# Kernel optimization log

Measured on AMD Instinct MI355X. Metric: run time of the kernel, lower is better.

## Reference

```python
import jax, jax.numpy as jnp
import numpy as np

B, P = 16, 4096            # clouds, points per cloud (N = B*P)
RATIO = 0.25
M = int(P * RATIO)          # FPS samples per cloud = 1024
K = 16                      # num_neighbors
F_IN, F_OUT = 64, 128
BN_EPS = 1e-5


def setup_inputs() -> dict:
    key = jax.random.key(0)
    k1, k2, k3 = jax.random.split(key, 3)
    position = jax.random.normal(k1, (B * P, 3), jnp.float32)
    features = jax.random.normal(k2, (B * P, F_IN), jnp.float32)
    batch_indices = jnp.repeat(jnp.arange(B, dtype=jnp.int32), P)  # sorted, equal-sized clouds
    W = jax.random.normal(k3, (F_IN, F_OUT), jnp.float32) * 0.05
    b = jnp.zeros((F_OUT,), jnp.float32)
    gamma = jnp.ones((F_OUT,), jnp.float32)
    beta = jnp.zeros((F_OUT,), jnp.float32)
    return {"position": position, "features": features, "batch_indices": batch_indices,
            "W": W, "b": b, "gamma": gamma, "beta": beta}


def _fps(pos):
    """Farthest point sampling on one cloud. pos: [P,3] -> indices [M].
    Deterministic start at index 0 (torch_cluster uses a random start)."""
    def step(carry, _):
        dist, last = carry
        d = jnp.sum((pos - pos[last]) ** 2, axis=-1)      # [P]
        dist = jnp.minimum(dist, d)                        # min dist to selected set
        nxt = jnp.argmax(dist).astype(jnp.int32)
        return (dist, nxt), nxt
    init = (jnp.full((P,), jnp.inf, pos.dtype), jnp.int32(0))
    _, idx = jax.lax.scan(step, init, None, length=M - 1)
    return jnp.concatenate([jnp.zeros((1,), jnp.int32), idx])


def _knn(x, q):
    """k nearest neighbors of queries q [M,F] among x [P,F] (feature space!). -> [M,K] indices."""
    d2 = (jnp.sum(q * q, -1, keepdims=True) - 2.0 * q @ x.T + jnp.sum(x * x, -1))  # [M,P]
    _, idx = jax.lax.top_k(-d2, K)
    return idx


def reference(position, features, batch_indices, W, b, gamma, beta):
    pos = position.reshape(B, P, 3)
    feat = features.reshape(B, P, F_IN)

    # FPS on positions (per cloud)
    fps_idx = jax.vmap(_fps)(pos)                                   # [B,M]

    # MLP: Linear + BatchNorm1d (training-mode batch stats over all N) + ReLU
    h = features @ W + b                                            # [N,F_OUT]
    mean = jnp.mean(h, axis=0)
    var = jnp.var(h, axis=0)
    h = jax.nn.relu((h - mean) * jax.lax.rsqrt(var + BN_EPS) * gamma + beta)
    h = h.reshape(B, P, F_OUT)

    # KNN in feature space: queries are features at FPS indices
    q = jnp.take_along_axis(feat, fps_idx[..., None], axis=1)       # [B,M,F_IN]
    nbr = jax.vmap(_knn)(feat, q)                                   # [B,M,K]

    # gather transformed features of neighbors and max-pool per query
    nbr_feats = jax.vmap(lambda hb, ib: hb[ib])(h, nbr)             # [B,M,K,F_OUT]
    new_features = jnp.max(nbr_feats, axis=2).reshape(B * M, F_OUT)

    new_position = jnp.take_along_axis(pos, fps_idx[..., None], axis=1).reshape(B * M, 3)
    new_batch = jnp.repeat(jnp.arange(B, dtype=batch_indices.dtype), M)
    return new_features, new_position, new_batch
```

## Files before the change

### kernel.cpp

```cpp
#include <hip/hip_runtime.h>
#include <hip/hip_bf16.h>

#define NB 16
#define NP 4096
#define MS 1024
#define NN 65536
#define FIN 64
#define FOUT 128
#define KNN_MARGIN 0.25f

typedef __attribute__((ext_vector_type(8))) short short8;
typedef __attribute__((ext_vector_type(4))) float f32x4;
typedef __attribute__((ext_vector_type(2))) float f32x2;

template <int CTRL>
__device__ __forceinline__ unsigned long long dpp_fmax_step(unsigned long long k) {
    unsigned lo = (unsigned)k, hi = (unsigned)(k >> 32);
    unsigned plo = (unsigned)__builtin_amdgcn_update_dpp(0, (int)lo, CTRL, 0xf, 0xf, true);
    unsigned phi = (unsigned)__builtin_amdgcn_update_dpp(0, (int)hi, CTRL, 0xf, 0xf, true);
    unsigned long long pk = ((unsigned long long)phi << 32) | plo;
    double a = __builtin_bit_cast(double, k);
    double p = __builtin_bit_cast(double, pk);
    return __builtin_bit_cast(unsigned long long, fmax(a, p));
}

__device__ __forceinline__ unsigned short bf16_rn(float v) {
    unsigned u = __float_as_uint(v);
    unsigned r = u + 0x7FFF + ((u >> 16) & 1);
    return (unsigned short)(r >> 16);
}


__global__ __launch_bounds__(512, 1) void front_kernel(
        const float* __restrict__ pos, const float* __restrict__ feat,
        const float* __restrict__ W, const float* __restrict__ bias,
        int* __restrict__ fps_idx, float* __restrict__ out_pos, float* __restrict__ out_batch,
        float* __restrict__ xnorm, unsigned short* __restrict__ Xt,
        __hip_bfloat16* __restrict__ hout, float* __restrict__ gsum, float* __restrict__ gsq) {
    __shared__ __align__(16) char smraw[69760];
    const int t = threadIdx.x;
    const int b = blockIdx.x;
    if (b < 16) {
        float4* plds4 = (float4*)smraw;
        float*  plin  = (float*)smraw;
        int* idxL = (int*)(smraw + 65536);
        double* wk = (double*)(smraw + 65536 + 4096);
        const float* pb = pos + (size_t)b * NP * 3;
#pragma unroll
        for (int i = 0; i < 24; i++) { int id = t + 512 * i; plin[id] = pb[id]; }
        __syncthreads();
        f32x2 px2[4], py2[4], pz2[4], dist2[4];
#pragma unroll
        for (int j = 0; j < 4; j++) {
            int p0 = t + 512 * (2 * j), p1 = p0 + 512;
            px2[j] = {plin[p0 * 3 + 0], plin[p1 * 3 + 0]};
            py2[j] = {plin[p0 * 3 + 1], plin[p1 * 3 + 1]};
            pz2[j] = {plin[p0 * 3 + 2], plin[p1 * 3 + 2]};
            dist2[j] = {INFINITY, INFINITY};
        }
        __syncthreads();
#pragma unroll
        for (int j = 0; j < 4; j++) {
            plds4[t + 512 * (2 * j)]     = (float4){px2[j][0], py2[j][0], pz2[j][0], 0.f};
            plds4[t + 512 * (2 * j + 1)] = (float4){px2[j][1], py2[j][1], pz2[j][1], 0.f};
        }
        if (t == 0) idxL[0] = 0;
        __syncthreads();
        float4 c0 = plds4[0];
        float lx = c0.x, ly = c0.y, lz = c0.z;
        const int ln = t & 63, wv = t >> 6;
        for (int m = 1; m < MS; m++) {
#pragma unroll
            for (int j = 0; j < 4; j++) {
                f32x2 dx = px2[j] - lx, dy = py2[j] - ly, dz = pz2[j] - lz;
                f32x2 d = dx * dx + dy * dy + dz * dz;
                dist2[j] = __builtin_elementwise_min(dist2[j], d);
            }
            float d1[4]; int i1[4];
#pragma unroll
            for (int j = 0; j < 4; j++) {
                bool g = dist2[j][1] > dist2[j][0];
                d1[j] = g ? dist2[j][1] : dist2[j][0];
                i1[j] = 2 * j + (g ? 1 : 0);
            }
            float d2[2]; int i2[2];
#pragma unroll
            for (int j = 0; j < 2; j++) {
                bool g = d1[j + 2] > d1[j];
                d2[j] = g ? d1[j + 2] : d1[j]; i2[j] = g ? i1[j + 2] : i1[j];
            }
            bool g3 = d2[1] > d2[0];
            float bd = g3 ? d2[1] : d2[0];
            int bi = g3 ? i2[1] : i2[0];
            int bp = t + (bi << 9);
            unsigned long long key =
                ((unsigned long long)__float_as_uint(bd) << 32) | (unsigned)(~bp);
            key = dpp_fmax_step<0x111>(key);
            key = dpp_fmax_step<0x112>(key);
            key = dpp_fmax_step<0x114>(key);
            key = dpp_fmax_step<0x118>(key);
            key = dpp_fmax_step<0x142>(key);
            key = dpp_fmax_step<0x143>(key);
            const int par = (m & 1) * 8;
            if (ln == 63) wk[par + wv] = __builtin_bit_cast(double, key);
            __syncthreads();
            const double2* wk2 = (const double2*)(wk + par);
            double2 q01 = wk2[0], q23 = wk2[1], q45 = wk2[2], q67 = wk2[3];
            double ka = fmax(q01.x, q01.y), kb = fmax(q23.x, q23.y);
            double kc = fmax(q45.x, q45.y), kd = fmax(q67.x, q67.y);
            ka = fmax(ka, kb);
            kc = fmax(kc, kd);
            unsigned long long kw = __builtin_bit_cast(unsigned long long, fmax(ka, kc));
            bp = (int)(~(unsigned)kw) & 0xFFF;
            float4 c = plds4[bp];
            lx = c.x; ly = c.y; lz = c.z;
            if (t == 0) idxL[m] = bp;
        }
        __syncthreads();
        for (int m = t; m < MS; m += 512) {
            int ix = idxL[m];
            size_t o = (size_t)b * MS + m;
            fps_idx[o] = ix;
            float4 c = plds4[ix];
            out_pos[o * 3 + 0] = c.x;
            out_pos[o * 3 + 1] = c.y;
            out_pos[o * 3 + 2] = c.z;
            out_batch[o] = (float)b;
        }
    } else if (b < 272) {
        float* wt = (float*)smraw;
        float* fl = (float*)smraw + 8704;
#pragma unroll
        for (int it = 0; it < 4; it++) {
            int lid = t + 512 * it;
            int k = lid >> 5, c4 = lid & 31;
            float4 v = *(const float4*)&W[k * FOUT + c4 * 4];
            wt[(c4 * 4 + 0) * 68 + k] = v.x;
            wt[(c4 * 4 + 1) * 68 + k] = v.y;
            wt[(c4 * 4 + 2) * 68 + k] = v.z;
            wt[(c4 * 4 + 3) * 68 + k] = v.w;
        }
        const int rowbase0 = (b - 16) * 256;
        const int rg = t >> 5, cg = t & 31;
        float sums[4] = {0, 0, 0, 0};
        float sqs[4]  = {0, 0, 0, 0};
        for (int sub = 0; sub < 4; sub++) {
            const int rowbase = rowbase0 + sub * 64;
            __syncthreads();
#pragma unroll
            for (int it = 0; it < 2; it++) {
                int lid = t + 512 * it;
                int r = lid >> 4, f4 = lid & 15;
                float4 v = *(const float4*)&feat[(size_t)(rowbase + r) * FIN + f4 * 4];
                *(float4*)&fl[r * 68 + f4 * 4] = v;
            }
            __syncthreads();
            float acc[4][4];
#pragma unroll
            for (int i = 0; i < 4; i++)
#pragma unroll
                for (int j = 0; j < 4; j++) acc[i][j] = 0.f;
#pragma unroll 2
            for (int k4 = 0; k4 < 16; k4++) {
                float4 f4v[4], w4v[4];
#pragma unroll
                for (int i = 0; i < 4; i++) f4v[i] = *(float4*)&fl[(rg * 4 + i) * 68 + k4 * 4];
#pragma unroll
                for (int j = 0; j < 4; j++) w4v[j] = *(float4*)&wt[(cg + 32 * j) * 68 + k4 * 4];
#pragma unroll
                for (int i = 0; i < 4; i++)
#pragma unroll
                    for (int j = 0; j < 4; j++) {
                        acc[i][j] = fmaf(f4v[i].x, w4v[j].x, acc[i][j]);
                        acc[i][j] = fmaf(f4v[i].y, w4v[j].y, acc[i][j]);
                        acc[i][j] = fmaf(f4v[i].z, w4v[j].z, acc[i][j]);
                        acc[i][j] = fmaf(f4v[i].w, w4v[j].w, acc[i][j]);
                    }
            }
#pragma unroll
            for (int j = 0; j < 4; j++) {
                int c = cg + 32 * j;
                float bc = bias[c];
#pragma unroll
                for (int i = 0; i < 4; i++) {
                    float h = acc[i][j] + bc;
                    sums[j] += h; sqs[j] += h * h;
                    hout[(size_t)(rowbase + rg * 4 + i) * FOUT + c] = __float2bfloat16(h);
                }
            }
        }
        __syncthreads();
        float* suml = fl;
        float* sql  = wt;
#pragma unroll
        for (int j = 0; j < 4; j++) {
            suml[rg * FOUT + cg + 32 * j] = sums[j];
            sql[rg * FOUT + cg + 32 * j]  = sqs[j];
        }
        __syncthreads();
        if (t < FOUT) {
            float S = 0.f, Q = 0.f;
#pragma unroll
            for (int r = 0; r < 16; r++) { S += suml[r * FOUT + t]; Q += sql[r * FOUT + t]; }
            atomicAdd(&gsum[t], S);
            atomicAdd(&gsq[t], Q);
        }
    } else {
        int r = (b - 272) * 512 + t;
        const float4* fr = (const float4*)&feat[(size_t)r * FIN];
        unsigned short hrow[64], lrow[64];
        float s = 0.f;
#pragma unroll
        for (int i = 0; i < 16; i++) {
            float4 v = fr[i];
            s += v.x * v.x + v.y * v.y + v.z * v.z + v.w * v.w;
            float vv[4] = {v.x, v.y, v.z, v.w};
#pragma unroll
            for (int j = 0; j < 4; j++) {
                unsigned short h = bf16_rn(vv[j]);
                float hf = __uint_as_float((unsigned)h << 16);
                hrow[4 * i + j] = h;
                lrow[4 * i + j] = bf16_rn(vv[j] - hf);
            }
        }
        xnorm[r] = s;
        const size_t tbase = (size_t)(r >> 4) * 2048;
        const int col = r & 15;
#pragma unroll
        for (int q = 0; q < 4; q++) {
            short8 f0, f1, f2, f3;
#pragma unroll
            for (int j = 0; j < 8; j++) {
                f0[j] = (short)hrow[q * 8 + j];
                f1[j] = (short)hrow[32 + q * 8 + j];
                f2[j] = (short)lrow[q * 8 + j];
                f3[j] = (short)lrow[32 + q * 8 + j];
            }
            const int ch = (q * 16 + col) * 8;
            *(short8*)&Xt[tbase + ch]        = f0;
            *(short8*)&Xt[tbase + 512 + ch]  = f1;
            *(short8*)&Xt[tbase + 1024 + ch] = f2;
            *(short8*)&Xt[tbase + 1536 + ch] = f3;
        }
    }
}

#define KNN_LOAD(SLOT_H0, SLOT_H1, SLOT_L0, SLOT_L1, SLOT_XN, TILE)                     \
    {                                                                                   \
        const unsigned short* tb_ = Xt + (size_t)(gtbase + (TILE)) * 2048;              \
        SLOT_H0 = *(const short8*)(tb_ + lane * 8);                                     \
        SLOT_H1 = *(const short8*)(tb_ + 512 + lane * 8);                               \
        SLOT_L0 = *(const short8*)(tb_ + 1024 + lane * 8);                              \
        SLOT_L1 = *(const short8*)(tb_ + 1536 + lane * 8);                              \
        SLOT_XN = xnorm[cbase + pstart + (TILE) * 16 + col];                            \
    }

#define KNN_MFMA(ACC, H0, H1, L0, L1)                                                   \
    ACC = __builtin_amdgcn_mfma_f32_16x16x32_bf16(Ah0, H0, ACC, 0, 0, 0);               \
    ACC = __builtin_amdgcn_mfma_f32_16x16x32_bf16(Ah1, H1, ACC, 0, 0, 0);               \
    ACC = __builtin_amdgcn_mfma_f32_16x16x32_bf16(Al0, H0, ACC, 0, 0, 0);               \
    ACC = __builtin_amdgcn_mfma_f32_16x16x32_bf16(Al1, H1, ACC, 0, 0, 0);               \
    ACC = __builtin_amdgcn_mfma_f32_16x16x32_bf16(Ah0, L0, ACC, 0, 0, 0);               \
    ACC = __builtin_amdgcn_mfma_f32_16x16x32_bf16(Ah1, L1, ACC, 0, 0, 0);

__global__ __launch_bounds__(256, 2) void knn_kernel(
        const unsigned short* __restrict__ Xt,
        const int* __restrict__ fps_idx, const float* __restrict__ xnorm,
        unsigned short* __restrict__ cand) {
    __shared__ float TL[4][16][32];
    __shared__ float TQ[4][16];
    __shared__ int   cntL[4][16];
    __shared__ unsigned short buf[4][16][64];
    const int t = threadIdx.x, b = blockIdx.x;
    const int cloud = b & 15, qg = (b >> 4) & 15, half = b >> 8;
    const int wave = t >> 6, lane = t & 63;
    const int quad = lane >> 4, col = lane & 15;
    const int cbase = cloud * NP;
    const int qloc = qg * 64 + wave * 16;
    const int pstart = half * 2048;
    const int gtbase = cloud * 256 + half * 128;

    const int qrow = fps_idx[cloud * MS + qloc + col];
    const unsigned short* qt = Xt + (size_t)(cloud * 256 + (qrow >> 4)) * 2048
                               + (size_t)((quad << 4) | (qrow & 15)) * 8;
    short8 Ah0 = *(const short8*)(qt);
    short8 Ah1 = *(const short8*)(qt + 512);
    short8 Al0 = *(const short8*)(qt + 1024);
    short8 Al1 = *(const short8*)(qt + 1536);

    float mA[4] = {INFINITY, INFINITY, INFINITY, INFINITY};
    float mB[4] = {INFINITY, INFINITY, INFINITY, INFINITY};
    {
        short8 ah0, ah1, al0, al1; float axn;
        short8 bh0, bh1, bl0, bl1; float bxn;
        KNN_LOAD(ah0, ah1, al0, al1, axn, 0)
        KNN_LOAD(bh0, bh1, bl0, bl1, bxn, 1)
        for (int tt = 0; tt < 128; tt += 2) {
            {
                f32x4 acc = {0.f, 0.f, 0.f, 0.f};
                KNN_MFMA(acc, ah0, ah1, al0, al1)
                float xnv = axn;
                if (tt + 2 < 128) KNN_LOAD(ah0, ah1, al0, al1, axn, tt + 2)
#pragma unroll
                for (int r = 0; r < 4; r++) {
                    float s = fmaf(-2.0f, acc[r], xnv);
                    float mx = fmaxf(mA[r], s);
                    mA[r] = fminf(mA[r], s);
                    mB[r] = fminf(mB[r], mx);
                }
            }
            {
                f32x4 acc = {0.f, 0.f, 0.f, 0.f};
                KNN_MFMA(acc, bh0, bh1, bl0, bl1)
                float xnv = bxn;
                if (tt + 3 < 128) KNN_LOAD(bh0, bh1, bl0, bl1, bxn, tt + 3)
#pragma unroll
                for (int r = 0; r < 4; r++) {
                    float s = fmaf(-2.0f, acc[r], xnv);
                    float mx = fmaxf(mA[r], s);
                    mA[r] = fminf(mA[r], s);
                    mB[r] = fminf(mB[r], mx);
                }
            }
        }
    }
#pragma unroll
    for (int r = 0; r < 4; r++) {
        TL[wave][quad * 4 + r][col * 2 + 0] = mA[r];
        TL[wave][quad * 4 + r][col * 2 + 1] = mB[r];
    }
    if (lane < 16) cntL[wave][lane] = 0;
    {
        const int q = lane >> 2, j0 = (lane & 3) * 8;
        float v[32];
#pragma unroll
        for (int j = 0; j < 32; j++) v[j] = TL[wave][q][j];
#pragma unroll
        for (int u = 0; u < 8; u++) {
            float vj = TL[wave][q][j0 + u];
            int jj = j0 + u, rank = 0;
#pragma unroll
            for (int k = 0; k < 32; k++)
                rank += (v[k] < vj || (v[k] == vj && k < jj)) ? 1 : 0;
            if (rank == 15) TQ[wave][q] = vj;
        }
    }
    float T0 = TQ[wave][quad * 4 + 0] + KNN_MARGIN;
    float T1 = TQ[wave][quad * 4 + 1] + KNN_MARGIN;
    float T2 = TQ[wave][quad * 4 + 2] + KNN_MARGIN;
    float T3 = TQ[wave][quad * 4 + 3] + KNN_MARGIN;
    {
        short8 ah0, ah1, al0, al1; float axn;
        short8 bh0, bh1, bl0, bl1; float bxn;
        KNN_LOAD(ah0, ah1, al0, al1, axn, 0)
        KNN_LOAD(bh0, bh1, bl0, bl1, bxn, 1)
        for (int tt = 0; tt < 128; tt += 2) {
            {
                f32x4 acc = {0.f, 0.f, 0.f, 0.f};
                KNN_MFMA(acc, ah0, ah1, al0, al1)
                float xnv = axn;
                if (tt + 2 < 128) KNN_LOAD(ah0, ah1, al0, al1, axn, tt + 2)
                const int pidx = pstart + tt * 16 + col;
                float s0 = fmaf(-2.0f, acc[0], xnv);
                float s1 = fmaf(-2.0f, acc[1], xnv);
                float s2 = fmaf(-2.0f, acc[2], xnv);
                float s3 = fmaf(-2.0f, acc[3], xnv);
                if (s0 <= T0) { int p = atomicAdd(&cntL[wave][quad * 4 + 0], 1); if (p < 64) buf[wave][quad * 4 + 0][p] = (unsigned short)pidx; }
                if (s1 <= T1) { int p = atomicAdd(&cntL[wave][quad * 4 + 1], 1); if (p < 64) buf[wave][quad * 4 + 1][p] = (unsigned short)pidx; }
                if (s2 <= T2) { int p = atomicAdd(&cntL[wave][quad * 4 + 2], 1); if (p < 64) buf[wave][quad * 4 + 2][p] = (unsigned short)pidx; }
                if (s3 <= T3) { int p = atomicAdd(&cntL[wave][quad * 4 + 3], 1); if (p < 64) buf[wave][quad * 4 + 3][p] = (unsigned short)pidx; }
            }
            {
                f32x4 acc = {0.f, 0.f, 0.f, 0.f};
                KNN_MFMA(acc, bh0, bh1, bl0, bl1)
                float xnv = bxn;
                if (tt + 3 < 128) KNN_LOAD(bh0, bh1, bl0, bl1, bxn, tt + 3)
                const int pidx = pstart + (tt + 1) * 16 + col;
                float s0 = fmaf(-2.0f, acc[0], xnv);
                float s1 = fmaf(-2.0f, acc[1], xnv);
                float s2 = fmaf(-2.0f, acc[2], xnv);
                float s3 = fmaf(-2.0f, acc[3], xnv);
                if (s0 <= T0) { int p = atomicAdd(&cntL[wave][quad * 4 + 0], 1); if (p < 64) buf[wave][quad * 4 + 0][p] = (unsigned short)pidx; }
                if (s1 <= T1) { int p = atomicAdd(&cntL[wave][quad * 4 + 1], 1); if (p < 64) buf[wave][quad * 4 + 1][p] = (unsigned short)pidx; }
                if (s2 <= T2) { int p = atomicAdd(&cntL[wave][quad * 4 + 2], 1); if (p < 64) buf[wave][quad * 4 + 2][p] = (unsigned short)pidx; }
                if (s3 <= T3) { int p = atomicAdd(&cntL[wave][quad * 4 + 3], 1); if (p < 64) buf[wave][quad * 4 + 3][p] = (unsigned short)pidx; }
            }
        }
    }
#pragma unroll
    for (int q = 0; q < 16; q++) {
        int n = cntL[wave][q];
        unsigned short val = (lane < n) ? buf[wave][q][lane] : (unsigned short)0xFFFF;
        cand[(size_t)(cloud * MS + qloc + q) * 128 + half * 64 + lane] = val;
    }
}

__global__ __launch_bounds__(256) void refine_kernel(
        const float* __restrict__ feat, const int* __restrict__ fps_idx,
        const float* __restrict__ xnorm, const unsigned short* __restrict__ cand,
        const __hip_bfloat16* __restrict__ h,
        const float* __restrict__ gsum, const float* __restrict__ gsq,
        const float* __restrict__ gamma, const float* __restrict__ beta,
        float* __restrict__ out_feat) {
    __shared__ float qlds[64];
    __shared__ __align__(16) int2 cDI[128];
    __shared__ int   rankH[128];
    __shared__ int   fIdx[16];
    __shared__ float cf[256];
    __shared__ float pmax[128];
    const int t = threadIdx.x, b = blockIdx.x;
    const int cloud = b & 15, m = b >> 4;
    const int q = cloud * MS + m;
    const int cbase = cloud * NP;
    if (t < 128) {
        float mean = gsum[t] * (1.0f / NN);
        float var  = gsq[t] * (1.0f / NN) - mean * mean;
        float s = rsqrtf(var + 1e-5f) * gamma[t];
        cf[t] = s;
        cf[128 + t] = beta[t] - mean * s;
    }
    if (t < 16) {
        int qr = fps_idx[q];
        float4 v = ((const float4*)(feat + (size_t)(cbase + qr) * FIN))[t];
        *(float4*)&qlds[t * 4] = v;
    }
    __syncthreads();
    const int c = t >> 1, jh = t & 1;
    const unsigned short cs = cand[(size_t)q * 128 + c];
    const bool valid = (cs != 0xFFFF);
    const int cidx = valid ? (int)cs : 0;
    const float4* xr = (const float4*)(feat + (size_t)(cbase + cidx) * FIN) + jh * 8;
    float a0 = 0.f, a1 = 0.f, a2 = 0.f, a3 = 0.f;
#pragma unroll
    for (int i = 0; i < 8; i++) {
        float4 x4 = xr[i];
        a0 = fmaf(qlds[jh * 32 + 4 * i + 0], x4.x, a0);
        a1 = fmaf(qlds[jh * 32 + 4 * i + 1], x4.y, a1);
        a2 = fmaf(qlds[jh * 32 + 4 * i + 2], x4.z, a2);
        a3 = fmaf(qlds[jh * 32 + 4 * i + 3], x4.w, a3);
    }
    float a = (a0 + a1) + (a2 + a3);
    a += __shfl_xor(a, 1);
    if (jh == 0) {
        float dv = valid ? fmaf(-2.0f, a, xnorm[cbase + cidx]) : INFINITY;
        int   iv = valid ? cidx : (65536 + c);
        cDI[c] = make_int2(__float_as_int(dv), iv);
    }
    __syncthreads();
    {
        const int c2 = t & 127, jH = t >> 7;
        int2 my = cDI[c2];
        float dv = __int_as_float(my.x);
        int   iv = my.y;
        const int4* cDI4 = (const int4*)cDI;
        int rank = 0;
        const int base = jH * 32;
#pragma unroll 8
        for (int k2 = 0; k2 < 32; k2++) {
            int4 p = cDI4[base + k2];
            float d0 = __int_as_float(p.x); int i0 = p.y;
            float d1 = __int_as_float(p.z); int i1 = p.w;
            rank += (d0 < dv || (d0 == dv && i0 < iv)) ? 1 : 0;
            rank += (d1 < dv || (d1 == dv && i1 < iv)) ? 1 : 0;
        }
        if (jH) rankH[c2] = rank;
        __syncthreads();
        if (!jH) {
            rank += rankH[c2];
            if (rank < 16) fIdx[rank] = iv;
        }
    }
    __syncthreads();
    {
        const int tc = t & 127, kH = t >> 7;
        const __hip_bfloat16* hb = h + (size_t)cbase * FOUT;
        const float ac = cf[tc], cc = cf[128 + tc];
        float mx = -INFINITY;
#pragma unroll
        for (int k = 0; k < 8; k++) {
            int row = fIdx[kH * 8 + k];
            float hv = __bfloat162float(hb[(size_t)row * FOUT + tc]);
            mx = fmaxf(mx, fmaxf(fmaf(ac, hv, cc), 0.f));
        }
        if (kH) pmax[tc] = mx;
        __syncthreads();
        if (!kH) out_feat[(size_t)q * FOUT + tc] = fmaxf(mx, pmax[tc]);
    }
}

extern "C" void kernel_launch(void* const* d_in, const int* in_sizes, int n_in,
                              void* d_out, int out_size, void* d_ws, size_t ws_size,
                              hipStream_t stream) {
    (void)in_sizes; (void)n_in; (void)out_size; (void)ws_size;
    const float* position = (const float*)d_in[0];
    const float* features = (const float*)d_in[1];
    const float* W        = (const float*)d_in[3];
    const float* bias     = (const float*)d_in[4];
    const float* gamma    = (const float*)d_in[5];
    const float* beta     = (const float*)d_in[6];
    float* out = (float*)d_out;

    char* ws = (char*)d_ws;
    int*   fps_idx = (int*)ws;
    float* gsum    = (float*)(ws + 65536);
    float* gsq     = (float*)(ws + 66048);
    float* xnorm   = (float*)(ws + 67584);
    unsigned short* cand = (unsigned short*)(ws + 329728);
    unsigned short* Xt   = (unsigned short*)(ws + 4524032);
    __hip_bfloat16* hbuf = (__hip_bfloat16*)(ws + 21301248);

    float* out_feat  = out;
    float* out_pos   = out + 2097152;
    float* out_batch = out + 2146304;

    hipMemsetAsync(gsum, 0, 1024, stream);
    front_kernel<<<400, 512, 0, stream>>>(position, features, W, bias,
                                          fps_idx, out_pos, out_batch, xnorm, Xt,
                                          hbuf, gsum, gsq);
    knn_kernel<<<512, 256, 0, stream>>>(Xt, fps_idx, xnorm, cand);
    refine_kernel<<<16384, 256, 0, stream>>>(features, fps_idx, xnorm, cand,
                                             hbuf, gsum, gsq, gamma, beta, out_feat);
}
```

Before: 759.0 us.

## Fuse front and KNN kernels with FPS progress flags to overlap KNN with FPS

Merges the FPS/MLP/split-bf16 front kernel and the KNN candidate kernel into one persistent launch of 256 blocks. The 16 FPS blocks publish selected indices every 64 samples through agent-scope release flags. The other blocks first build Xt and run the MLP tiles, then start KNN query tasks as soon as the matching FPS prefix is ready. This hides the serial FPS latency behind KNN and MLP work instead of running KNN only after it ends. The cost is spin-waiting on global flags and a reliance on all 256 blocks being co-resident to avoid deadlock.

```diff
diff --git a/kernel.cpp b/kernel.cpp
--- a/kernel.cpp
+++ b/kernel.cpp
@@ -31,12 +31,31 @@
 }
 
 
-__global__ __launch_bounds__(512, 1) void front_kernel(
+#define KNN_LOAD(SLOT_H0, SLOT_H1, SLOT_L0, SLOT_L1, SLOT_XN, TILE)                     \
+    {                                                                                   \
+        const unsigned short* tb_ = Xt + (size_t)(gtbase + (TILE)) * 2048;              \
+        SLOT_H0 = *(const short8*)(tb_ + lane * 8);                                     \
+        SLOT_H1 = *(const short8*)(tb_ + 512 + lane * 8);                               \
+        SLOT_L0 = *(const short8*)(tb_ + 1024 + lane * 8);                              \
+        SLOT_L1 = *(const short8*)(tb_ + 1536 + lane * 8);                              \
+        SLOT_XN = xnorm[cbase + pstart + (TILE) * 16 + col];                            \
+    }
+
+#define KNN_MFMA(ACC, H0, H1, L0, L1)                                                   \
+    ACC = __builtin_amdgcn_mfma_f32_16x16x32_bf16(Ah0, H0, ACC, 0, 0, 0);               \
+    ACC = __builtin_amdgcn_mfma_f32_16x16x32_bf16(Ah1, H1, ACC, 0, 0, 0);               \
+    ACC = __builtin_amdgcn_mfma_f32_16x16x32_bf16(Al0, H0, ACC, 0, 0, 0);               \
+    ACC = __builtin_amdgcn_mfma_f32_16x16x32_bf16(Al1, H1, ACC, 0, 0, 0);               \
+    ACC = __builtin_amdgcn_mfma_f32_16x16x32_bf16(Ah0, L0, ACC, 0, 0, 0);               \
+    ACC = __builtin_amdgcn_mfma_f32_16x16x32_bf16(Ah1, L1, ACC, 0, 0, 0);
+
+__global__ __launch_bounds__(512) void fused_kernel(
         const float* __restrict__ pos, const float* __restrict__ feat,
         const float* __restrict__ W, const float* __restrict__ bias,
         int* __restrict__ fps_idx, float* __restrict__ out_pos, float* __restrict__ out_batch,
         float* __restrict__ xnorm, unsigned short* __restrict__ Xt,
-        __hip_bfloat16* __restrict__ hout, float* __restrict__ gsum, float* __restrict__ gsq) {
+        __hip_bfloat16* __restrict__ hout, float* __restrict__ gsum, float* __restrict__ gsq,
+        unsigned short* __restrict__ cand, int* __restrict__ ready, int* __restrict__ sdone) {
     __shared__ __align__(16) char smraw[69760];
     const int t = threadIdx.x;
     const int b = blockIdx.x;
@@ -64,7 +83,7 @@
             plds4[t + 512 * (2 * j)]     = (float4){px2[j][0], py2[j][0], pz2[j][0], 0.f};
             plds4[t + 512 * (2 * j + 1)] = (float4){px2[j][1], py2[j][1], pz2[j][1], 0.f};
         }
-        if (t == 0) idxL[0] = 0;
+        if (t == 0) { idxL[0] = 0; fps_idx[(size_t)b * MS] = 0; }
         __syncthreads();
         float4 c0 = plds4[0];
         float lx = c0.x, ly = c0.y, lz = c0.z;
@@ -114,284 +133,284 @@
             bp = (int)(~(unsigned)kw) & 0xFFF;
             float4 c = plds4[bp];
             lx = c.x; ly = c.y; lz = c.z;
-            if (t == 0) idxL[m] = bp;
+            if (t == 0) {
+                idxL[m] = bp;
+                fps_idx[(size_t)b * MS + m] = bp;
+                if ((m & 63) == 63) {
+                    __threadfence();
+                    __hip_atomic_store(&ready[b], m + 1, __ATOMIC_RELEASE,
+                                       __HIP_MEMORY_SCOPE_AGENT);
+                }
+            }
         }
         __syncthreads();
         for (int m = t; m < MS; m += 512) {
             int ix = idxL[m];
             size_t o = (size_t)b * MS + m;
-            fps_idx[o] = ix;
             float4 c = plds4[ix];
             out_pos[o * 3 + 0] = c.x;
             out_pos[o * 3 + 1] = c.y;
             out_pos[o * 3 + 2] = c.z;
             out_batch[o] = (float)b;
         }
-    } else if (b < 272) {
-        float* wt = (float*)smraw;
-        float* fl = (float*)smraw + 8704;
-#pragma unroll
-        for (int it = 0; it < 4; it++) {
-            int lid = t + 512 * it;
-            int k = lid >> 5, c4 = lid & 31;
-            float4 v = *(const float4*)&W[k * FOUT + c4 * 4];
-            wt[(c4 * 4 + 0) * 68 + k] = v.x;
-            wt[(c4 * 4 + 1) * 68 + k] = v.y;
-            wt[(c4 * 4 + 2) * 68 + k] = v.z;
-            wt[(c4 * 4 + 3) * 68 + k] = v.w;
-        }
-        const int rowbase0 = (b - 16) * 256;
-        const int rg = t >> 5, cg = t & 31;
-        float sums[4] = {0, 0, 0, 0};
-        float sqs[4]  = {0, 0, 0, 0};
-        for (int sub = 0; sub < 4; sub++) {
-            const int rowbase = rowbase0 + sub * 64;
+    } else {
+        const int w = b - 16;
+        if (w < 128) {
+            int r = w * 512 + t;
+            const float4* fr = (const float4*)&feat[(size_t)r * FIN];
+            unsigned short hrow[64], lrow[64];
+            float s = 0.f;
+#pragma unroll
+            for (int i = 0; i < 16; i++) {
+                float4 v = fr[i];
+                s += v.x * v.x + v.y * v.y + v.z * v.z + v.w * v.w;
+                float vv[4] = {v.x, v.y, v.z, v.w};
+#pragma unroll
+                for (int j = 0; j < 4; j++) {
+                    unsigned short h = bf16_rn(vv[j]);
+                    float hf = __uint_as_float((unsigned)h << 16);
+                    hrow[4 * i + j] = h;
+                    lrow[4 * i + j] = bf16_rn(vv[j] - hf);
+                }
+            }
+            xnorm[r] = s;
+            const size_t tbase = (size_t)(r >> 4) * 2048;
+            const int col = r & 15;
+#pragma unroll
+            for (int q = 0; q < 4; q++) {
+                short8 f0, f1, f2, f3;
+#pragma unroll
+                for (int j = 0; j < 8; j++) {
+                    f0[j] = (short)hrow[q * 8 + j];
+                    f1[j] = (short)hrow[32 + q * 8 + j];
+                    f2[j] = (short)lrow[q * 8 + j];
+                    f3[j] = (short)lrow[32 + q * 8 + j];
+                }
+                const int ch = (q * 16 + col) * 8;
+                *(short8*)&Xt[tbase + ch]        = f0;
+                *(short8*)&Xt[tbase + 512 + ch]  = f1;
+                *(short8*)&Xt[tbase + 1024 + ch] = f2;
+                *(short8*)&Xt[tbase + 1536 + ch] = f3;
+            }
+            __threadfence();
+        }
+        __syncthreads();
+        if (w < 128 && t == 0)
+            __hip_atomic_fetch_add(sdone, 1, __ATOMIC_RELEASE, __HIP_MEMORY_SCOPE_AGENT);
+        for (int tile = w; tile < 256; tile += 240) {
+            float* wt = (float*)smraw;
+            float* fl = (float*)smraw + 8704;
+#pragma unroll
+            for (int it = 0; it < 4; it++) {
+                int lid = t + 512 * it;
+                int k = lid >> 5, c4 = lid & 31;
+                float4 v = *(const float4*)&W[k * FOUT + c4 * 4];
+                wt[(c4 * 4 + 0) * 68 + k] = v.x;
+                wt[(c4 * 4 + 1) * 68 + k] = v.y;
+                wt[(c4 * 4 + 2) * 68 + k] = v.z;
+                wt[(c4 * 4 + 3) * 68 + k] = v.w;
+            }
+            const int rowbase0 = tile * 256;
+            const int rg = t >> 5, cg = t & 31;
+            float sums[4] = {0, 0, 0, 0};
+            float sqs[4]  = {0, 0, 0, 0};
+            for (int sub = 0; sub < 4; sub++) {
+                const int rowbase = rowbase0 + sub * 64;
+                __syncthreads();
+#pragma unroll
+                for (int it = 0; it < 2; it++) {
+                    int lid = t + 512 * it;
+                    int r = lid >> 4, f4 = lid & 15;
+                    float4 v = *(const float4*)&feat[(size_t)(rowbase + r) * FIN + f4 * 4];
+                    *(float4*)&fl[r * 68 + f4 * 4] = v;
+                }
+                __syncthreads();
+                float acc[4][4];
+#pragma unroll
+                for (int i = 0; i < 4; i++)
+#pragma unroll
+                    for (int j = 0; j < 4; j++) acc[i][j] = 0.f;
+#pragma unroll 2
+                for (int k4 = 0; k4 < 16; k4++) {
+                    float4 f4v[4], w4v[4];
+#pragma unroll
+                    for (int i = 0; i < 4; i++) f4v[i] = *(float4*)&fl[(rg * 4 + i) * 68 + k4 * 4];
+#pragma unroll
+                    for (int j = 0; j < 4; j++) w4v[j] = *(float4*)&wt[(cg + 32 * j) * 68 + k4 * 4];
+#pragma unroll
+                    for (int i = 0; i < 4; i++)
+#pragma unroll
+                        for (int j = 0; j < 4; j++) {
+                            acc[i][j] = fmaf(f4v[i].x, w4v[j].x, acc[i][j]);
+                            acc[i][j] = fmaf(f4v[i].y, w4v[j].y, acc[i][j]);
+                            acc[i][j] = fmaf(f4v[i].z, w4v[j].z, acc[i][j]);
+                            acc[i][j] = fmaf(f4v[i].w, w4v[j].w, acc[i][j]);
+                        }
+                }
+#pragma unroll
+                for (int j = 0; j < 4; j++) {
+                    int c = cg + 32 * j;
+                    float bc = bias[c];
+#pragma unroll
+                    for (int i = 0; i < 4; i++) {
+                        float h = acc[i][j] + bc;
+                        sums[j] += h; sqs[j] += h * h;
+                        hout[(size_t)(rowbase + rg * 4 + i) * FOUT + c] = __float2bfloat16(h);
+                    }
+                }
+            }
             __syncthreads();
-#pragma unroll
-            for (int it = 0; it < 2; it++) {
-                int lid = t + 512 * it;
-                int r = lid >> 4, f4 = lid & 15;
-                float4 v = *(const float4*)&feat[(size_t)(rowbase + r) * FIN + f4 * 4];
-                *(float4*)&fl[r * 68 + f4 * 4] = v;
+            float* suml = fl;
+            float* sql  = wt;
+#pragma unroll
+            for (int j = 0; j < 4; j++) {
+                suml[rg * FOUT + cg + 32 * j] = sums[j];
+                sql[rg * FOUT + cg + 32 * j]  = sqs[j];
             }
             __syncthreads();
-            float acc[4][4];
-#pragma unroll
-            for (int i = 0; i < 4; i++)
-#pragma unroll
-                for (int j = 0; j < 4; j++) acc[i][j] = 0.f;
-#pragma unroll 2
-            for (int k4 = 0; k4 < 16; k4++) {
-                float4 f4v[4], w4v[4];
-#pragma unroll
-                for (int i = 0; i < 4; i++) f4v[i] = *(float4*)&fl[(rg * 4 + i) * 68 + k4 * 4];
-#pragma unroll
-                for (int j = 0; j < 4; j++) w4v[j] = *(float4*)&wt[(cg + 32 * j) * 68 + k4 * 4];
-#pragma unroll
-                for (int i = 0; i < 4; i++)
-#pragma unroll
-                    for (int j = 0; j < 4; j++) {
-                        acc[i][j] = fmaf(f4v[i].x, w4v[j].x, acc[i][j]);
-                        acc[i][j] = fmaf(f4v[i].y, w4v[j].y, acc[i][j]);
-                        acc[i][j] = fmaf(f4v[i].z, w4v[j].z, acc[i][j]);
-                        acc[i][j] = fmaf(f4v[i].w, w4v[j].w, acc[i][j]);
+            if (t < FOUT) {
+                float S = 0.f, Q = 0.f;
+#pragma unroll
+                for (int r = 0; r < 16; r++) { S += suml[r * FOUT + t]; Q += sql[r * FOUT + t]; }
+                atomicAdd(&gsum[t], S);
+                atomicAdd(&gsq[t], Q);
+            }
+            __syncthreads();
+        }
+        float (*TL)[16][32] = (float(*)[16][32])smraw;
+        float (*TQ)[16]     = (float(*)[16])(smraw + 16384);
+        int   (*cntL)[16]   = (int(*)[16])(smraw + 16896);
+        unsigned short (*bufL)[16][64] = (unsigned short(*)[16][64])(smraw + 17408);
+        const int wave = t >> 6, lane = t & 63;
+        const int quad = lane >> 4, col = lane & 15;
+        while (__hip_atomic_load(sdone, __ATOMIC_ACQUIRE, __HIP_MEMORY_SCOPE_AGENT) < 128)
+            __builtin_amdgcn_s_sleep(64);
+        auto knn_task = [&](int tid) {
+            const int cloud = tid & 15;
+            const int half  = (tid >> 4) & 1;
+            const int qloc  = (tid >> 5) * 16;
+            const int cbase = cloud * NP;
+            const int pstart = half * 2048;
+            const int gtbase = cloud * 256 + half * 128;
+            const int need = qloc + 16;
+            while (__hip_atomic_load(&ready[cloud], __ATOMIC_ACQUIRE,
+                                     __HIP_MEMORY_SCOPE_AGENT) < need)
+                __builtin_amdgcn_s_sleep(64);
+            const int qrow = fps_idx[cloud * MS + qloc + col];
+            const unsigned short* qt = Xt + (size_t)(cloud * 256 + (qrow >> 4)) * 2048
+                                       + (size_t)((quad << 4) | (qrow & 15)) * 8;
+            short8 Ah0 = *(const short8*)(qt);
+            short8 Ah1 = *(const short8*)(qt + 512);
+            short8 Al0 = *(const short8*)(qt + 1024);
+            short8 Al1 = *(const short8*)(qt + 1536);
+            float mA[4] = {INFINITY, INFINITY, INFINITY, INFINITY};
+            float mB[4] = {INFINITY, INFINITY, INFINITY, INFINITY};
+            {
+                short8 ah0, ah1, al0, al1; float axn;
+                short8 bh0, bh1, bl0, bl1; float bxn;
+                KNN_LOAD(ah0, ah1, al0, al1, axn, 0)
+                KNN_LOAD(bh0, bh1, bl0, bl1, bxn, 1)
+                for (int tt = 0; tt < 128; tt += 2) {
+                    {
+                        f32x4 acc = {0.f, 0.f, 0.f, 0.f};
+                        KNN_MFMA(acc, ah0, ah1, al0, al1)
+                        float xnv = axn;
+                        if (tt + 2 < 128) KNN_LOAD(ah0, ah1, al0, al1, axn, tt + 2)
+#pragma unroll
+                        for (int r = 0; r < 4; r++) {
+                            float s = fmaf(-2.0f, acc[r], xnv);
+                            float mx = fmaxf(mA[r], s);
+                            mA[r] = fminf(mA[r], s);
+                            mB[r] = fminf(mB[r], mx);
+                        }
                     }
-            }
-#pragma unroll
-            for (int j = 0; j < 4; j++) {
-                int c = cg + 32 * j;
-                float bc = bias[c];
-#pragma unroll
-                for (int i = 0; i < 4; i++) {
-                    float h = acc[i][j] + bc;
-                    sums[j] += h; sqs[j] += h * h;
-                    hout[(size_t)(rowbase + rg * 4 + i) * FOUT + c] = __float2bfloat16(h);
-                }
-            }
-        }
-        __syncthreads();
-        float* suml = fl;
-        float* sql  = wt;
-#pragma unroll
-        for (int j = 0; j < 4; j++) {
-            suml[rg * FOUT + cg + 32 * j] = sums[j];
-            sql[rg * FOUT + cg + 32 * j]  = sqs[j];
-        }
-        __syncthreads();
-        if (t < FOUT) {
-            float S = 0.f, Q = 0.f;
-#pragma unroll
-            for (int r = 0; r < 16; r++) { S += suml[r * FOUT + t]; Q += sql[r * FOUT + t]; }
-            atomicAdd(&gsum[t], S);
-            atomicAdd(&gsq[t], Q);
-        }
-    } else {
-        int r = (b - 272) * 512 + t;
-        const float4* fr = (const float4*)&feat[(size_t)r * FIN];
-        unsigned short hrow[64], lrow[64];
-        float s = 0.f;
-#pragma unroll
-        for (int i = 0; i < 16; i++) {
-            float4 v = fr[i];
-            s += v.x * v.x + v.y * v.y + v.z * v.z + v.w * v.w;
-            float vv[4] = {v.x, v.y, v.z, v.w};
-#pragma unroll
-            for (int j = 0; j < 4; j++) {
-                unsigned short h = bf16_rn(vv[j]);
-                float hf = __uint_as_float((unsigned)h << 16);
-                hrow[4 * i + j] = h;
-                lrow[4 * i + j] = bf16_rn(vv[j] - hf);
-            }
-        }
-        xnorm[r] = s;
-        const size_t tbase = (size_t)(r >> 4) * 2048;
-        const int col = r & 15;
-#pragma unroll
-        for (int q = 0; q < 4; q++) {
-            short8 f0, f1, f2, f3;
-#pragma unroll
-            for (int j = 0; j < 8; j++) {
-                f0[j] = (short)hrow[q * 8 + j];
-                f1[j] = (short)hrow[32 + q * 8 + j];
-                f2[j] = (short)lrow[q * 8 + j];
-                f3[j] = (short)lrow[32 + q * 8 + j];
-            }
-            const int ch = (q * 16 + col) * 8;
-            *(short8*)&Xt[tbase + ch]        = f0;
-            *(short8*)&Xt[tbase + 512 + ch]  = f1;
-            *(short8*)&Xt[tbase + 1024 + ch] = f2;
-            *(short8*)&Xt[tbase + 1536 + ch] = f3;
-        }
-    }
-}
-
-#define KNN_LOAD(SLOT_H0, SLOT_H1, SLOT_L0, SLOT_L1, SLOT_XN, TILE)                     \
-    {                                                                                   \
-        const unsigned short* tb_ = Xt + (size_t)(gtbase + (TILE)) * 2048;              \
-        SLOT_H0 = *(const short8*)(tb_ + lane * 8);                                     \
-        SLOT_H1 = *(const short8*)(tb_ + 512 + lane * 8);                               \
-        SLOT_L0 = *(const short8*)(tb_ + 1024 + lane * 8);                              \
-        SLOT_L1 = *(const short8*)(tb_ + 1536 + lane * 8);                              \
-        SLOT_XN = xnorm[cbase + pstart + (TILE) * 16 + col];                            \
-    }
-
-#define KNN_MFMA(ACC, H0, H1, L0, L1)                                                   \
-    ACC = __builtin_amdgcn_mfma_f32_16x16x32_bf16(Ah0, H0, ACC, 0, 0, 0);               \
-    ACC = __builtin_amdgcn_mfma_f32_16x16x32_bf16(Ah1, H1, ACC, 0, 0, 0);               \
-    ACC = __builtin_amdgcn_mfma_f32_16x16x32_bf16(Al0, H0, ACC, 0, 0, 0);               \
-    ACC = __builtin_amdgcn_mfma_f32_16x16x32_bf16(Al1, H1, ACC, 0, 0, 0);               \
-    ACC = __builtin_amdgcn_mfma_f32_16x16x32_bf16(Ah0, L0, ACC, 0, 0, 0);               \
-    ACC = __builtin_amdgcn_mfma_f32_16x16x32_bf16(Ah1, L1, ACC, 0, 0, 0);
-
-__global__ __launch_bounds__(256, 2) void knn_kernel(
-        const unsigned short* __restrict__ Xt,
-        const int* __restrict__ fps_idx, const float* __restrict__ xnorm,
-        unsigned short* __restrict__ cand) {
-    __shared__ float TL[4][16][32];
-    __shared__ float TQ[4][16];
-    __shared__ int   cntL[4][16];
-    __shared__ unsigned short buf[4][16][64];
-    const int t = threadIdx.x, b = blockIdx.x;
-    const int cloud = b & 15, qg = (b >> 4) & 15, half = b >> 8;
-    const int wave = t >> 6, lane = t & 63;
-    const int quad = lane >> 4, col = lane & 15;
-    const int cbase = cloud * NP;
-    const int qloc = qg * 64 + wave * 16;
-    const int pstart = half * 2048;
-    const int gtbase = cloud * 256 + half * 128;
-
-    const int qrow = fps_idx[cloud * MS + qloc + col];
-    const unsigned short* qt = Xt + (size_t)(cloud * 256 + (qrow >> 4)) * 2048
-                               + (size_t)((quad << 4) | (qrow & 15)) * 8;
-    short8 Ah0 = *(const short8*)(qt);
-    short8 Ah1 = *(const short8*)(qt + 512);
-    short8 Al0 = *(const short8*)(qt + 1024);
-    short8 Al1 = *(const short8*)(qt + 1536);
-
-    float mA[4] = {INFINITY, INFINITY, INFINITY, INFINITY};
-    float mB[4] = {INFINITY, INFINITY, INFINITY, INFINITY};
-    {
-        short8 ah0, ah1, al0, al1; float axn;
-        short8 bh0, bh1, bl0, bl1; float bxn;
-        KNN_LOAD(ah0, ah1, al0, al1, axn, 0)
-        KNN_LOAD(bh0, bh1, bl0, bl1, bxn, 1)
-        for (int tt = 0; tt < 128; tt += 2) {
+                    {
+                        f32x4 acc = {0.f, 0.f, 0.f, 0.f};
+                        KNN_MFMA(acc, bh0, bh1, bl0, bl1)
+                        float xnv = bxn;
+                        if (tt + 3 < 128) KNN_LOAD(bh0, bh1, bl0, bl1, bxn, tt + 3)
+#pragma unroll
+                        for (int r = 0; r < 4; r++) {
+                            float s = fmaf(-2.0f, acc[r], xnv);
+                            float mx = fmaxf(mA[r], s);
+                            mA[r] = fminf(mA[r], s);
+                            mB[r] = fminf(mB[r], mx);
+                        }
+                    }
+                }
+            }
+#pragma unroll
+            for (int r = 0; r < 4; r++) {
+                TL[wave][quad * 4 + r][col * 2 + 0] = mA[r];
+                TL[wave][quad * 4 + r][col * 2 + 1] = mB[r];
+            }
+            if (lane < 16) cntL[wave][lane] = 0;
             {
-                f32x4 acc = {0.f, 0.f, 0.f, 0.f};
-                KNN_MFMA(acc, ah0, ah1, al0, al1)
-                float xnv = axn;
-                if (tt + 2 < 128) KNN_LOAD(ah0, ah1, al0, al1, axn, tt + 2)
-#pragma unroll
-                for (int r = 0; r < 4; r++) {
-                    float s = fmaf(-2.0f, acc[r], xnv);
-                    float mx = fmaxf(mA[r], s);
-                    mA[r] = fminf(mA[r], s);
-                    mB[r] = fminf(mB[r], mx);
-                }
-            }
+                const int q = lane >> 2, j0 = (lane & 3) * 8;
+                float v[32];
+#pragma unroll
+                for (int j = 0; j < 32; j++) v[j] = TL[wave][q][j];
+#pragma unroll
+                for (int u = 0; u < 8; u++) {
+                    float vj = TL[wave][q][j0 + u];
+                    int jj = j0 + u, rank = 0;
+#pragma unroll
+                    for (int k = 0; k < 32; k++)
+                        rank += (v[k] < vj || (v[k] == vj && k < jj)) ? 1 : 0;
+                    if (rank == 15) TQ[wave][q] = vj;
+                }
+            }
+            float T0 = TQ[wave][quad * 4 + 0] + KNN_MARGIN;
+            float T1 = TQ[wave][quad * 4 + 1] + KNN_MARGIN;
+            float T2 = TQ[wave][quad * 4 + 2] + KNN_MARGIN;
+            float T3 = TQ[wave][quad * 4 + 3] + KNN_MARGIN;
             {
-                f32x4 acc = {0.f, 0.f, 0.f, 0.f};
-                KNN_MFMA(acc, bh0, bh1, bl0, bl1)
-                float xnv = bxn;
-                if (tt + 3 < 128) KNN_LOAD(bh0, bh1, bl0, bl1, bxn, tt + 3)
-#pragma unroll
-                for (int r = 0; r < 4; r++) {
-                    float s = fmaf(-2.0f, acc[r], xnv);
-                    float mx = fmaxf(mA[r], s);
-                    mA[r] = fminf(mA[r], s);
-                    mB[r] = fminf(mB[r], mx);
-                }
-            }
-        }
-    }
-#pragma unroll
-    for (int r = 0; r < 4; r++) {
-        TL[wave][quad * 4 + r][col * 2 + 0] = mA[r];
-        TL[wave][quad * 4 + r][col * 2 + 1] = mB[r];
-    }
-    if (lane < 16) cntL[wave][lane] = 0;
-    {
-        const int q = lane >> 2, j0 = (lane & 3) * 8;
-        float v[32];
-#pragma unroll
-        for (int j = 0; j < 32; j++) v[j] = TL[wave][q][j];
-#pragma unroll
-        for (int u = 0; u < 8; u++) {
-            float vj = TL[wave][q][j0 + u];
-            int jj = j0 + u, rank = 0;
-#pragma unroll
-            for (int k = 0; k < 32; k++)
-                rank += (v[k] < vj || (v[k] == vj && k < jj)) ? 1 : 0;
-            if (rank == 15) TQ[wave][q] = vj;
-        }
-    }
-    float T0 = TQ[wave][quad * 4 + 0] + KNN_MARGIN;
-    float T1 = TQ[wave][quad * 4 + 1] + KNN_MARGIN;
-    float T2 = TQ[wave][quad * 4 + 2] + KNN_MARGIN;
-    float T3 = TQ[wave][quad * 4 + 3] + KNN_MARGIN;
-    {
-        short8 ah0, ah1, al0, al1; float axn;
-        short8 bh0, bh1, bl0, bl1; float bxn;
-        KNN_LOAD(ah0, ah1, al0, al1, axn, 0)
-        KNN_LOAD(bh0, bh1, bl0, bl1, bxn, 1)
-        for (int tt = 0; tt < 128; tt += 2) {
-            {
-                f32x4 acc = {0.f, 0.f, 0.f, 0.f};
-                KNN_MFMA(acc, ah0, ah1, al0, al1)
-                float xnv = axn;
-                if (tt + 2 < 128) KNN_LOAD(ah0, ah1, al0, al1, axn, tt + 2)
-                const int pidx = pstart + tt * 16 + col;
-                float s0 = fmaf(-2.0f, acc[0], xnv);
-                float s1 = fmaf(-2.0f, acc[1], xnv);
-                float s2 = fmaf(-2.0f, acc[2], xnv);
-                float s3 = fmaf(-2.0f, acc[3], xnv);
-                if (s0 <= T0) { int p = atomicAdd(&cntL[wave][quad * 4 + 0], 1); if (p < 64) buf[wave][quad * 4 + 0][p] = (unsigned short)pidx; }
-                if (s1 <= T1) { int p = atomicAdd(&cntL[wave][quad * 4 + 1], 1); if (p < 64) buf[wave][quad * 4 + 1][p] = (unsigned short)pidx; }
-                if (s2 <= T2) { int p = atomicAdd(&cntL[wave][quad * 4 + 2], 1); if (p < 64) buf[wave][quad * 4 + 2][p] = (unsigned short)pidx; }
-                if (s3 <= T3) { int p = atomicAdd(&cntL[wave][quad * 4 + 3], 1); if (p < 64) buf[wave][quad * 4 + 3][p] = (unsigned short)pidx; }
-            }
-            {
-                f32x4 acc = {0.f, 0.f, 0.f, 0.f};
-                KNN_MFMA(acc, bh0, bh1, bl0, bl1)
-                float xnv = bxn;
-                if (tt + 3 < 128) KNN_LOAD(bh0, bh1, bl0, bl1, bxn, tt + 3)
-                const int pidx = pstart + (tt + 1) * 16 + col;
-                float s0 = fmaf(-2.0f, acc[0], xnv);
-                float s1 = fmaf(-2.0f, acc[1], xnv);
-                float s2 = fmaf(-2.0f, acc[2], xnv);
-                float s3 = fmaf(-2.0f, acc[3], xnv);
-                if (s0 <= T0) { int p = atomicAdd(&cntL[wave][quad * 4 + 0], 1); if (p < 64) buf[wave][quad * 4 + 0][p] = (unsigned short)pidx; }
-                if (s1 <= T1) { int p = atomicAdd(&cntL[wave][quad * 4 + 1], 1); if (p < 64) buf[wave][quad * 4 + 1][p] = (unsigned short)pidx; }
-                if (s2 <= T2) { int p = atomicAdd(&cntL[wave][quad * 4 + 2], 1); if (p < 64) buf[wave][quad * 4 + 2][p] = (unsigned short)pidx; }
-                if (s3 <= T3) { int p = atomicAdd(&cntL[wave][quad * 4 + 3], 1); if (p < 64) buf[wave][quad * 4 + 3][p] = (unsigned short)pidx; }
-            }
-        }
-    }
-#pragma unroll
-    for (int q = 0; q < 16; q++) {
-        int n = cntL[wave][q];
-        unsigned short val = (lane < n) ? buf[wave][q][lane] : (unsigned short)0xFFFF;
-        cand[(size_t)(cloud * MS + qloc + q) * 128 + half * 64 + lane] = val;
+                short8 ah0, ah1, al0, al1; float axn;
+                short8 bh0, bh1, bl0, bl1; float bxn;
+                KNN_LOAD(ah0, ah1, al0, al1, axn, 0)
+                KNN_LOAD(bh0, bh1, bl0, bl1, bxn, 1)
+                for (int tt = 0; tt < 128; tt += 2) {
+                    {
+                        f32x4 acc = {0.f, 0.f, 0.f, 0.f};
+                        KNN_MFMA(acc, ah0, ah1, al0, al1)
+                        float xnv = axn;
+                        if (tt + 2 < 128) KNN_LOAD(ah0, ah1, al0, al1, axn, tt + 2)
+                        const int pidx = pstart + tt * 16 + col;
+                        float s0 = fmaf(-2.0f, acc[0], xnv);
+                        float s1 = fmaf(-2.0f, acc[1], xnv);
+                        float s2 = fmaf(-2.0f, acc[2], xnv);
+                        float s3 = fmaf(-2.0f, acc[3], xnv);
+                        if (s0 <= T0) { int p = atomicAdd(&cntL[wave][quad * 4 + 0], 1); if (p < 64) bufL[wave][quad * 4 + 0][p] = (unsigned short)pidx; }
+                        if (s1 <= T1) { int p = atomicAdd(&cntL[wave][quad * 4 + 1], 1); if (p < 64) bufL[wave][quad * 4 + 1][p] = (unsigned short)pidx; }
+                        if (s2 <= T2) { int p = atomicAdd(&cntL[wave][quad * 4 + 2], 1); if (p < 64) bufL[wave][quad * 4 + 2][p] = (unsigned short)pidx; }
+                        if (s3 <= T3) { int p = atomicAdd(&cntL[wave][quad * 4 + 3], 1); if (p < 64) bufL[wave][quad * 4 + 3][p] = (unsigned short)pidx; }
+                    }
+                    {
+                        f32x4 acc = {0.f, 0.f, 0.f, 0.f};
+                        KNN_MFMA(acc, bh0, bh1, bl0, bl1)
+                        float xnv = bxn;
+                        if (tt + 3 < 128) KNN_LOAD(bh0, bh1, bl0, bl1, bxn, tt + 3)
+                        const int pidx = pstart + (tt + 1) * 16 + col;
+                        float s0 = fmaf(-2.0f, acc[0], xnv);
+                        float s1 = fmaf(-2.0f, acc[1], xnv);
+                        float s2 = fmaf(-2.0f, acc[2], xnv);
+                        float s3 = fmaf(-2.0f, acc[3], xnv);
+                        if (s0 <= T0) { int p = atomicAdd(&cntL[wave][quad * 4 + 0], 1); if (p < 64) bufL[wave][quad * 4 + 0][p] = (unsigned short)pidx; }
+                        if (s1 <= T1) { int p = atomicAdd(&cntL[wave][quad * 4 + 1], 1); if (p < 64) bufL[wave][quad * 4 + 1][p] = (unsigned short)pidx; }
+                        if (s2 <= T2) { int p = atomicAdd(&cntL[wave][quad * 4 + 2], 1); if (p < 64) bufL[wave][quad * 4 + 2][p] = (unsigned short)pidx; }
+                        if (s3 <= T3) { int p = atomicAdd(&cntL[wave][quad * 4 + 3], 1); if (p < 64) bufL[wave][quad * 4 + 3][p] = (unsigned short)pidx; }
+                    }
+                }
+            }
+#pragma unroll
+            for (int q = 0; q < 16; q++) {
+                int n = cntL[wave][q];
+                unsigned short val = (lane < n) ? bufL[wave][q][lane] : (unsigned short)0xFFFF;
+                cand[(size_t)(cloud * MS + qloc + q) * 128 + half * 64 + lane] = val;
+            }
+        };
+        knn_task(w * 8 + wave);
+        if (wave == 0 && w < 128) knn_task(1920 + w);
     }
 }
 
@@ -504,6 +523,8 @@
     int*   fps_idx = (int*)ws;
     float* gsum    = (float*)(ws + 65536);
     float* gsq     = (float*)(ws + 66048);
+    int*   ready   = (int*)(ws + 66560);
+    int*   sdone   = (int*)(ws + 66624);
     float* xnorm   = (float*)(ws + 67584);
     unsigned short* cand = (unsigned short*)(ws + 329728);
     unsigned short* Xt   = (unsigned short*)(ws + 4524032);
@@ -513,11 +534,10 @@
     float* out_pos   = out + 2097152;
     float* out_batch = out + 2146304;
 
-    hipMemsetAsync(gsum, 0, 1024, stream);
-    front_kernel<<<400, 512, 0, stream>>>(position, features, W, bias,
+    hipMemsetAsync(ws + 65536, 0, 2048, stream);
+    fused_kernel<<<256, 512, 0, stream>>>(position, features, W, bias,
                                           fps_idx, out_pos, out_batch, xnorm, Xt,
-                                          hbuf, gsum, gsq);
-    knn_kernel<<<512, 256, 0, stream>>>(Xt, fps_idx, xnorm, cand);
+                                          hbuf, gsum, gsq, cand, ready, sdone);
     refine_kernel<<<16384, 256, 0, stream>>>(features, fps_idx, xnorm, cand,
                                              hbuf, gsum, gsq, gamma, beta, out_feat);
 }
```

After: 787.6 us. +3.8%, slower.
